# Kernel tuning notes

Measured on AMD Instinct MI355X. Metric: run time of the kernel, lower is better.

The kernel has to match this reference:

```python
import jax, jax.numpy as jnp
import numpy as np

N, T, F = 4096, 24, 16          # nodes, seq_len, in_features
H = 128                          # temporal_hidden
NH, DO = 4, 32                   # gat num_heads, gat out_features (NH*DO == H)
SEM, PH = 64, 32                 # semantic hidden, predictor hidden
SLOPE = 0.2                      # leaky_relu negative slope
ADJ_P = 0.01                     # adjacency density


def setup_inputs() -> dict:
    key = jax.random.key(0)
    ks = jax.random.split(key, 40)
    f32 = jnp.float32

    def rn(k, shape, s=0.02):
        return jax.random.normal(k, shape, f32) * s

    features = jax.random.normal(ks[0], (N, T, F), f32)
    pos_adj = (jax.random.uniform(ks[1], (N, N)) < ADJ_P).astype(f32)
    neg_adj = (jax.random.uniform(ks[2], (N, N)) < ADJ_P).astype(f32)

    inp = dict(features=features, pos_adj=pos_adj, neg_adj=neg_adj)
    # GRU (torch layout: W_ih [3H,F], W_hh [3H,H], gate order r,z,n)
    inp['gru_Wih'] = rn(ks[3], (3 * H, F), 1.0 / np.sqrt(H))
    inp['gru_Whh'] = rn(ks[4], (3 * H, H), 1.0 / np.sqrt(H))
    inp['gru_bih'] = rn(ks[5], (3 * H,), 1.0 / np.sqrt(H))
    inp['gru_bhh'] = rn(ks[6], (3 * H,), 1.0 / np.sqrt(H))
    # GAT params (linear weights stored [in, out] so we use x @ W)
    i = 7
    for pre in ('pos', 'neg'):
        inp[pre + '_W'] = rn(ks[i], (H, NH * DO)); i += 1
        inp[pre + '_u'] = rn(ks[i], (NH, DO, 1), 1.0); i += 1
        inp[pre + '_v'] = rn(ks[i], (NH, DO, 1), 1.0); i += 1
        inp[pre + '_b'] = rn(ks[i], (1, NH * DO)); i += 1
        inp[pre + '_pW'] = rn(ks[i], (H, NH * DO)); i += 1
        inp[pre + '_pb'] = jnp.zeros((NH * DO,), f32)
    inp['self_W'] = rn(ks[i], (H, H)); i += 1
    inp['self_b'] = jnp.zeros((H,), f32)
    inp['mpos_W'] = rn(ks[i], (NH * DO, H)); i += 1
    inp['mpos_b'] = jnp.zeros((H,), f32)
    inp['mneg_W'] = rn(ks[i], (NH * DO, H)); i += 1
    inp['mneg_b'] = jnp.zeros((H,), f32)
    inp['sem_W1'] = rn(ks[i], (H, SEM)); i += 1
    inp['sem_b1'] = jnp.zeros((SEM,), f32)
    inp['sem_W2'] = rn(ks[i], (SEM, 1)); i += 1
    inp['pred_W1'] = rn(ks[i], (H, PH)); i += 1
    inp['pred_b1'] = jnp.zeros((PH,), f32)
    inp['pred_W2'] = rn(ks[i], (PH, 1)); i += 1
    inp['pred_b2'] = jnp.zeros((1,), f32)
    return inp


def _gru_last(x, Wih, Whh, bih, bhh):
    # x: [N, T, F] -> last hidden state [N, H]
    gi_all = jnp.einsum('ntf,gf->tng', x, Wih) + bih  # precompute input gates [T,N,3H]
    h0 = jnp.zeros((x.shape[0], Whh.shape[1]), x.dtype)

    def step(h, gi):
        gh = h @ Whh.T + bhh
        ir, iz, in_ = jnp.split(gi, 3, axis=-1)
        hr, hz, hn = jnp.split(gh, 3, axis=-1)
        r = jax.nn.sigmoid(ir + hr)
        z = jax.nn.sigmoid(iz + hz)
        n = jnp.tanh(in_ + r * hn)
        return (1.0 - z) * n + z * h, None

    h, _ = jax.lax.scan(step, h0, gi_all)
    return h


def _gat(x, adj, W, u, v, b, pW, pb):
    sup = (x @ W).reshape(-1, NH, DO).transpose(1, 0, 2)     # [NH, N, DO]
    f1 = jnp.matmul(sup, u).reshape(NH, 1, -1)               # [NH, 1, N]
    f2 = jnp.matmul(sup, v).reshape(NH, -1, 1)               # [NH, N, 1]
    w = jax.nn.leaky_relu(f1 + f2, SLOPE)                    # [NH, N, N]
    mw = w * adj                                             # mask
    rs = mw.sum(axis=2, keepdims=True)
    rs = jnp.where(rs == 0, jnp.ones_like(rs), rs)
    attn = mw / rs
    out = jnp.matmul(attn, sup).transpose(1, 0, 2).reshape(-1, NH * DO)
    return out + b + x @ pW + pb                             # bias + residual


def _pairnorm_si(x):
    x = x - x.mean(axis=0)
    rn = jnp.sqrt(1e-6 + (x * x).sum(axis=1, keepdims=True))
    return x / rn


def reference(features, pos_adj, neg_adj,
              gru_Wih, gru_Whh, gru_bih, gru_bhh,
              pos_W, pos_u, pos_v, pos_b, pos_pW, pos_pb,
              neg_W, neg_u, neg_v, neg_b, neg_pW, neg_pb,
              self_W, self_b, mpos_W, mpos_b, mneg_W, mneg_b,
              sem_W1, sem_b1, sem_W2,
              pred_W1, pred_b1, pred_W2, pred_b2):
    support = _gru_last(features, gru_Wih, gru_Whh, gru_bih, gru_bhh)  # [N, H]
    pos_sup = _gat(support, pos_adj, pos_W, pos_u, pos_v, pos_b, pos_pW, pos_pb)
    neg_sup = _gat(support, neg_adj, neg_W, neg_u, neg_v, neg_b, neg_pW, neg_pb)
    self_e = support @ self_W + self_b
    pos_e = pos_sup @ mpos_W + mpos_b
    neg_e = neg_sup @ mneg_W + mneg_b
    emb = jnp.stack([self_e, pos_e, neg_e], axis=1)          # [N, 3, H]
    w = jnp.tanh(emb @ sem_W1 + sem_b1) @ sem_W2             # [N, 3, 1]
    beta = jax.nn.softmax(w, axis=1)
    fused = (beta * emb).sum(axis=1)                          # [N, H]
    fused = _pairnorm_si(fused)
    h = jax.nn.relu(fused @ pred_W1 + pred_b1)               # dropout is eval no-op
    out = jax.nn.sigmoid(h @ pred_W2 + pred_b2).squeeze(-1)  # [N]
    return out
```

## Files before the change

kernel.cpp:

```cpp
#include <hip/hip_runtime.h>


#define NN 4096

typedef unsigned short u16;
typedef unsigned int   u32;
typedef unsigned long long u64;
typedef __attribute__((ext_vector_type(8))) short  short8;
typedef __attribute__((ext_vector_type(4))) float  float4v;

__device__ inline float bf2f(u16 u){ return __uint_as_float(((u32)u)<<16); }
__device__ inline u16 f2bf(float f){
  u32 x = __float_as_uint(f);
  return (u16)((x + 0x7fffu + ((x>>16)&1u))>>16);
}
__device__ inline float ldm(const void* p, int i, int bf){
  return bf ? bf2f(((const u16*)p)[i]) : ((const float*)p)[i];
}
__device__ inline u16 ldm16(const void* p, int i, int bf){
  return bf ? ((const u16*)p)[i] : f2bf(((const float*)p)[i]);
}
__device__ inline float fexp(float x){
  x = fminf(fmaxf(x,-80.f),80.f);
  return __builtin_amdgcn_exp2f(x*1.4426950408889634f);
}
__device__ inline float sigm_fast(float x){
  return __builtin_amdgcn_rcpf(1.f + __builtin_amdgcn_exp2f(-x*1.4426950408889634f));
}
__device__ inline float tanhf_(float x){
  float c = fminf(fmaxf(x,-15.f),15.f);
  float e = __builtin_amdgcn_exp2f(c*2.8853900817779268f);
  return (e-1.f)*__builtin_amdgcn_rcpf(e+1.f);
}
__device__ inline float4v mfma16(short8 a, short8 b, float4v c){
  return __builtin_amdgcn_mfma_f32_16x16x32_bf16(a,b,c,0,0,0);
}
__device__ inline int rdbf(const int* __restrict__ mflag){
  int b=0;
  #pragma unroll
  for (int k=0;k<16;k++) b|=mflag[k];
  return b;
}

__global__ __launch_bounds__(256) void k_detect(const u32* __restrict__ adj,
                                                int* __restrict__ mflag)
{
  __shared__ u32 w4[4];
  const int lane=threadIdx.x&63, wv=threadIdx.x>>6;
  int i = (blockIdx.x*256 + threadIdx.x)*4;
  uint4 v = *(const uint4*)(adj + i);
  u32 acc = (v.x | v.y | v.z | v.w) & 0xFFFFu;
  unsigned long long b = __ballot(acc != 0);
  if (lane==0) w4[wv] = (b!=0);
  __syncthreads();
  if (threadIdx.x==0) mflag[blockIdx.x] = (w4[0]|w4[1]|w4[2]|w4[3]) ? 1 : 0;
}

__global__ __launch_bounds__(256) void k_imp(
  const int* __restrict__ mflag,
  const void* gWih, const void* gWhh, const void* gbih, const void* gbhh,
  const void* posW, const void* posu, const void* posv, const void* posb,
  const void* pospW, const void* pospb,
  const void* negW, const void* negu, const void* negv, const void* negb,
  const void* negpW, const void* negpb,
  const void* selfW, const void* selfb, const void* mposW, const void* mposb,
  const void* mnegW, const void* mnegb,
  const void* semW1, const void* semb1, const void* semW2,
  const void* predW1, const void* predb1, const void* predW2, const void* predb2,
  u16* __restrict__ Wihb, u16* __restrict__ Whhb,
  u16* __restrict__ WT1,  u16* __restrict__ WT2,
  float* __restrict__ cbrz, float* __restrict__ cbin, float* __restrict__ cbhn,
  float* __restrict__ cuv,  float* __restrict__ cgb,  float* __restrict__ csb,
  float* __restrict__ cw1t, float* __restrict__ cb1,  float* __restrict__ cw2,
  float* __restrict__ cpw1t, float* __restrict__ cpb1, float* __restrict__ cpw2,
  float* __restrict__ cpb2, float* __restrict__ meanacc)
{
  const int bf = rdbf(mflag);
  int i = blockIdx.x*256 + threadIdx.x;
  if (i < 6144){ Wihb[i]=ldm16(gWih,i,bf); return; }  i-=6144;
  if (i < 49152){ Whhb[i]=ldm16(gWhh,i,bf); return; } i-=49152;
  if (i < 81920){
    int m=i>>7,k=i&127,sel=m>>7,ml=m&127;
    const void* s = sel==0?posW: sel==1?pospW: sel==2?negW: sel==3?negpW: selfW;
    WT1[i]=ldm16(s,k*128+ml,bf); return;
  } i-=81920;
  if (i < 32768){
    int m=i>>7,k=i&127;
    const void* s = (m<128)? mposW : mnegW;
    WT2[i]=ldm16(s,k*128+(m&127),bf); return;
  } i-=32768;
  if (i < 256){ cbrz[i]=ldm(gbih,i,bf)+ldm(gbhh,i,bf); return; } i-=256;
  if (i < 128){ cbin[i]=ldm(gbih,256+i,bf); return; } i-=128;
  if (i < 128){ cbhn[i]=ldm(gbhh,256+i,bf); return; } i-=128;
  if (i < 512){
    int s=i>>8, rem=i&255, wh=rem>>7, hd=rem&127;
    const void* p = s? (wh? negv:negu) : (wh? posv:posu);
    cuv[i]=ldm(p,hd,bf); return;
  } i-=512;
  if (i < 256){
    int s=i>>7, d=i&127;
    cgb[i]=ldm(s?negb:posb,d,bf)+ldm(s?negpb:pospb,d,bf); return;
  } i-=256;
  if (i < 384){
    int t=i>>7, d=i&127;
    const void* p = t==0? selfb : t==1? mposb : mnegb;
    csb[i]=ldm(p,d,bf); return;
  } i-=384;
  if (i < 8448){
    int c=i/132, k=i-c*132;
    cw1t[i] = (k<128)? ldm(semW1,k*64+c,bf) : 0.f; return;
  } i-=8448;
  if (i < 64){ cb1[i]=ldm(semb1,i,bf); return; } i-=64;
  if (i < 64){ cw2[i]=ldm(semW2,i,bf); return; } i-=64;
  if (i < 4224){
    int c=i/132, k=i-c*132;
    cpw1t[i] = (k<128)? ldm(predW1,k*32+c,bf) : 0.f; return;
  } i-=4224;
  if (i < 32){ cpb1[i]=ldm(predb1,i,bf); return; } i-=32;
  if (i < 32){ cpw2[i]=ldm(predW2,i,bf); return; } i-=32;
  if (i < 1){ cpb2[i]=ldm(predb2,i,bf); return; } i-=1;
  if (i < 128){ meanacc[i]=0.f; return; }
}

__global__ __launch_bounds__(512) void k_gruf(
  const int* __restrict__ mflag, const void* feat,
  const u16* __restrict__ Wihb, const u16* __restrict__ Whhb,
  const float* __restrict__ cbrz, const float* __restrict__ cbin,
  const float* __restrict__ cbhn,
  const u16* __restrict__ WT1, const float* __restrict__ cuv,
  u16* __restrict__ C1b, float* __restrict__ f12)
{
  __shared__ __attribute__((aligned(16))) u16 sh_x[16*392];
  __shared__ __attribute__((aligned(16))) u16 hbuf[2][16*136];
  const int bf = rdbf(mflag);
  const int tid=threadIdx.x, lane=tid&63, wv=tid>>6;
  const int quad=lane>>4, c15=lane&15;
  const int n0=blockIdx.x*16;

  if (bf){
    const u16* f16p=(const u16*)feat;
    for (int i=tid;i<768;i+=512){
      int n=i/48, c=(i-n*48)*8;
      *(uint4*)(sh_x + n*392 + c) =
        *(const uint4*)(f16p + (size_t)(n0+n)*384 + c);
    }
  } else {
    const float* f32p=(const float*)feat;
    for (int i=tid;i<1536;i+=512){
      int n=i/96, c=(i-n*96)*4;
      float4 v = *(const float4*)(f32p + (size_t)(n0+n)*384 + c);
      uint2 pk;
      pk.x = (u32)f2bf(v.x) | ((u32)f2bf(v.y)<<16);
      pk.y = (u32)f2bf(v.z) | ((u32)f2bf(v.w)<<16);
      *(uint2*)(sh_x + n*392 + c) = pk;
    }
  }
  for (int i=tid;i<16*136;i+=512) hbuf[0][i]=0;

  const short8 z8={0,0,0,0,0,0,0,0};
  const float4v z4={0.f,0.f,0.f,0.f};
  short8 bh[3][4], bx3[3];
  #pragma unroll
  for (int g=0;g<3;g++){
    int rowb=(g*8+wv)*16+c15;
    #pragma unroll
    for (int ks=0;ks<4;ks++) bh[g][ks]=*(const short8*)(Whhb+(size_t)rowb*128+ks*32+quad*8);
    bx3[g] = (quad<2)? *(const short8*)(Wihb+(size_t)rowb*16+quad*8) : z8;
  }
  const int j0=wv*16+c15;
  const float brz_r=cbrz[j0], brz_z=cbrz[128+j0];
  const float bin0=cbin[j0],  bhn0=cbhn[j0];
  float hr[4]={0.f,0.f,0.f,0.f};
  __syncthreads();

  for (int t=0;t<24;t++){
    const u16* hb  = hbuf[t&1];
    u16*       hbn = hbuf[(t+1)&1];
    short8 ah[4];
    #pragma unroll
    for (int ks=0;ks<4;ks++) ah[ks]=*(const short8*)(hb + c15*136 + ks*32 + quad*8);
    short8 ax = (quad<2)? *(const short8*)(sh_x + c15*392 + t*16 + quad*8) : z8;
    float4v racc = mfma16(ax,bx3[0],z4);
    float4v zacc = mfma16(ax,bx3[1],z4);
    float4v ni   = mfma16(ax,bx3[2],z4);
    float4v nh   = z4;
    #pragma unroll
    for (int ks=0;ks<4;ks++){
      racc = mfma16(ah[ks],bh[0][ks],racc);
      zacc = mfma16(ah[ks],bh[1][ks],zacc);
      nh   = mfma16(ah[ks],bh[2][ks],nh);
    }
    #pragma unroll
    for (int rr=0;rr<4;rr++){
      const int node = quad*4+rr;
      float r_ = sigm_fast(racc[rr]+brz_r);
      float z_ = sigm_fast(zacc[rr]+brz_z);
      float n_ = tanhf_(ni[rr]+bin0 + r_*(nh[rr]+bhn0));
      float hv = (1.f-z_)*n_ + z_*hr[rr];
      hr[rr]=hv; hbn[node*136+j0]=f2bf(hv);
    }
    __syncthreads();
  }
  short8 a[4];
  #pragma unroll
  for (int ks=0;ks<4;ks++) a[ks]=*(const short8*)(hbuf[0]+c15*136+ks*32+quad*8);
  #pragma unroll
  for (int q=0;q<5;q++){
    int tile=wv*5+q;
    float4v acc={0.f,0.f,0.f,0.f};
    #pragma unroll
    for (int ks=0;ks<4;ks++){
      short8 b=*(const short8*)(WT1+(size_t)(tile*16+c15)*128+ks*32+quad*8);
      acc=mfma16(a[ks],b,acc);
    }
    #pragma unroll
    for (int r=0;r<4;r++)
      C1b[(size_t)(n0+quad*4+r)*640 + tile*16 + c15]=f2bf(acc[r]);
  }
  __syncthreads();
  {
    int q=tid;
    int nl=q&15, h=(q>>4)&3, wsel=(q>>6)&1, s=(q>>7)&1;
    const float* uvp = cuv + s*256 + wsel*128 + h*32;
    const u16*   SL  = C1b + (size_t)(n0+nl)*640 + s*256 + h*32;
    float t=0.f;
    #pragma unroll
    for (int d=0;d<32;d++) t += bf2f(SL[d])*uvp[d];
    f12[s*32768 + wsel*16384 + h*4096 + (n0+nl)] = t;
  }
}

__global__ __launch_bounds__(1024) void k_gat3(
  const int* __restrict__ mflag,
  const void* posadj, const void* negadj,
  const u16* __restrict__ C1b, const float* __restrict__ f12,
  const float* __restrict__ cgb, const u16* __restrict__ WT2,
  float* __restrict__ E)
{
  __shared__ u16   nbuf[16][128];
  __shared__ float wbuf[16][4][128];
  __shared__ __attribute__((aligned(16))) u16 sA[16*136];
  const int bf = rdbf(mflag);
  const int s=blockIdx.y;
  const void* adj = s? negadj : posadj;
  const int wv=threadIdx.x>>6, lane=threadIdx.x&63;
  const int n0=blockIdx.x*16;
  const int i=n0+wv;

  u64 mask=0;
  if (bf){
    const u16* rp = (const u16*)adj + (size_t)i*4096;
    #pragma unroll
    for (int it=0; it<8; it++){
      const uint4 vv = *(const uint4*)(rp + it*512 + lane*8);
      u32 w[4]={vv.x,vv.y,vv.z,vv.w};
      #pragma unroll
      for (int q=0;q<4;q++){
        if (w[q]&0xffffu) mask |= 1ull<<(it*8+2*q);
        if (w[q]>>16)     mask |= 1ull<<(it*8+2*q+1);
      }
    }
  } else {
    const float* rp = (const float*)adj + (size_t)i*4096;
    #pragma unroll
    for (int it=0; it<16; it++){
      const uint4 vv = *(const uint4*)(rp + it*256 + lane*4);
      if (vv.x) mask |= 1ull<<(it*4+0);
      if (vv.y) mask |= 1ull<<(it*4+1);
      if (vv.z) mask |= 1ull<<(it*4+2);
      if (vv.w) mask |= 1ull<<(it*4+3);
    }
  }
  int cnt=__popcll(mask);
  int pre=cnt;
  #pragma unroll
  for (int off=1; off<64; off<<=1){
    int o=__shfl_up(pre,off);
    if (lane>=off) pre+=o;
  }
  int base_p = pre-cnt;
  int total = __shfl(pre,63);
  const int dg = total>128 ? 128 : total;
  u64 mm=mask; int k=0;
  while (mm){
    int b=__ffsll(mm)-1; mm&=mm-1;
    int e = bf ? ((b>>3)*512 + lane*8 + (b&7))
               : ((b>>2)*256 + lane*4 + (b&3));
    int p=base_p+k; k++;
    if (p<128) nbuf[wv][p]=(u16)e;
  }

  const float* f1 = f12 + s*32768;
  const float* f2 = f12 + s*32768 + 16384;
  const int d0=lane, d1=lane+64, h0=lane>>5, h1=2+(lane>>5);
  float f2v[4];
  #pragma unroll
  for (int h=0;h<4;h++) f2v[h]=f2[h*4096+i];
  for (int e=lane; e<dg; e+=64){
    int j = nbuf[wv][e];
    #pragma unroll
    for (int h=0;h<4;h++){
      float w = f1[h*4096+j] + f2v[h];
      wbuf[wv][h][e] = w>0.f ? w : 0.2f*w;
    }
  }

  float acc0=0.f,acc1=0.f,rs0=0.f,rs1=0.f;
  #pragma unroll 4
  for (int e=0;e<dg;e++){
    float w0 = wbuf[wv][h0][e];
    float w1 = wbuf[wv][h1][e];
    int j = nbuf[wv][e];
    const u16* SL = C1b + (size_t)j*640 + s*256;
    acc0 += w0*bf2f(SL[d0]); rs0 += w0;
    acc1 += w1*bf2f(SL[d1]); rs1 += w1;
  }
  if (rs0==0.f) rs0=1.f;
  if (rs1==0.f) rs1=1.f;
  const u16* P = C1b + (size_t)i*640 + s*256 + 128;
  sA[wv*136+d0]=f2bf(acc0/rs0 + cgb[s*128+d0] + bf2f(P[d0]));
  sA[wv*136+d1]=f2bf(acc1/rs1 + cgb[s*128+d1] + bf2f(P[d1]));
  __syncthreads();
  if (wv<8){
    const int quad=lane>>4, c15=lane&15;
    short8 a[4];
    #pragma unroll
    for (int ks=0;ks<4;ks++) a[ks]=*(const short8*)(sA+c15*136+ks*32+quad*8);
    const int tile=wv;
    float4v acc={0.f,0.f,0.f,0.f};
    #pragma unroll
    for (int ks=0;ks<4;ks++){
      short8 b=*(const short8*)(WT2+(size_t)(s*128+tile*16+c15)*128+ks*32+quad*8);
      acc=mfma16(a[ks],b,acc);
    }
    #pragma unroll
    for (int r=0;r<4;r++) E[(size_t)(n0+quad*4+r)*256 + s*128 + tile*16 + c15]=acc[r];
  }
}

__global__ __launch_bounds__(256) void k_sem(
  const u16* __restrict__ C1b, const float* __restrict__ E,
  const float* __restrict__ csb, const float* __restrict__ cw1t,
  const float* __restrict__ cb1, const float* __restrict__ cw2,
  float* __restrict__ fused, float* __restrict__ meanacc)
{
  __shared__ float sW1t[64*132];
  __shared__ float sW2[64];
  __shared__ float sb1[64];
  __shared__ float sE[4][3][128];
  __shared__ float redm[4][128];
  const int tid=threadIdx.x, wv=tid>>6, lane=tid&63;
  for (int i=tid;i<8448;i+=256) sW1t[i]=cw1t[i];
  if (tid<64){ sW2[tid]=cw2[tid]; sb1[tid]=cb1[tid]; }
  __syncthreads();
  const float* wcol = sW1t + lane*132;
  float macc0=0.f, macc1=0.f;
  for (int u=0;u<4;u++){
    const int n = blockIdx.x*16 + wv*4 + u;
    for (int d=lane; d<128; d+=64){
      sE[wv][0][d] = bf2f(C1b[(size_t)n*640+512+d]) + csb[d];
      sE[wv][1][d] = E[(size_t)n*256 + d]    + csb[128+d];
      sE[wv][2][d] = E[(size_t)n*256+128+d]  + csb[256+d];
    }
    float sc[3];
    #pragma unroll
    for (int s=0;s<3;s++){
      float t = sb1[lane];
      #pragma unroll
      for (int k=0;k<128;k+=4){
        float4 e4 = *(const float4*)&sE[wv][s][k];
        float4 w4 = *(const float4*)&wcol[k];
        t += e4.x*w4.x + e4.y*w4.y + e4.z*w4.z + e4.w*w4.w;
      }
      t = tanhf_(t);
      float p = t*sW2[lane];
      #pragma unroll
      for (int off=32; off; off>>=1) p += __shfl_xor(p, off);
      sc[s]=p;
    }
    float mx = fmaxf(sc[0], fmaxf(sc[1],sc[2]));
    float e0=fexp(sc[0]-mx), e1=fexp(sc[1]-mx), e2=fexp(sc[2]-mx);
    float inv = 1.f/(e0+e1+e2);
    float b0=e0*inv, b1=e1*inv, b2=e2*inv;
    float f0 = b0*sE[wv][0][lane]    + b1*sE[wv][1][lane]    + b2*sE[wv][2][lane];
    float f1 = b0*sE[wv][0][lane+64] + b1*sE[wv][1][lane+64] + b2*sE[wv][2][lane+64];
    fused[(size_t)n*128+lane]    = f0;
    fused[(size_t)n*128+64+lane] = f1;
    macc0 += f0; macc1 += f1;
  }
  redm[wv][lane]=macc0; redm[wv][lane+64]=macc1;
  __syncthreads();
  if (tid<128)
    atomicAdd(&meanacc[tid], redm[0][tid]+redm[1][tid]+redm[2][tid]+redm[3][tid]);
}

__global__ __launch_bounds__(256) void k_pred(
  const float* __restrict__ fused, const float* __restrict__ meanacc,
  const float* __restrict__ cpw1t, const float* __restrict__ cpb1,
  const float* __restrict__ cpw2, const float* __restrict__ cpb2,
  float* __restrict__ out)
{
  __shared__ float sy[4][128];
  __shared__ float sW1t[32*132];
  __shared__ float sW2[32];
  const int tid=threadIdx.x, wv=tid>>6, lane=tid&63;
  for (int i=tid;i<4224;i+=256) sW1t[i]=cpw1t[i];
  if (tid<32) sW2[tid]=cpw2[tid];
  const int n = blockIdx.x*4 + wv;
  const float inv_n = 1.f/4096.f;
  float x0 = fused[(size_t)n*128+lane]    - meanacc[lane]*inv_n;
  float x1 = fused[(size_t)n*128+64+lane] - meanacc[64+lane]*inv_n;
  float ss = x0*x0 + x1*x1;
  #pragma unroll
  for (int o=32;o;o>>=1) ss += __shfl_xor(ss,o);
  float ir = 1.f/sqrtf(1e-6f + ss);
  sy[wv][lane]=x0*ir; sy[wv][64+lane]=x1*ir;
  __syncthreads();
  const int c = lane&31, half = lane>>5;
  const float* wcol = sW1t + c*132 + half*64;
  const float* yrow = sy[wv] + half*64;
  float h=0.f;
  #pragma unroll
  for (int k=0;k<64;k+=4){
    float4 y4 = *(const float4*)&yrow[k];
    float4 w4 = *(const float4*)&wcol[k];
    h += y4.x*w4.x + y4.y*w4.y + y4.z*w4.z + y4.w*w4.w;
  }
  h += __shfl_xor(h,32);
  h += cpb1[c];
  h = h>0.f? h : 0.f;
  float p = h*sW2[c];
  #pragma unroll
  for (int o=16;o;o>>=1) p += __shfl_xor(p,o);
  if (!lane){
    float z = p + cpb2[0];
    out[n] = __builtin_amdgcn_rcpf(1.f + fexp(-z));
  }
}

extern "C" void kernel_launch(void* const* d_in, const int* in_sizes, int n_in,
                              void* d_out, int out_size, void* d_ws, size_t ws_size,
                              hipStream_t stream)
{
  const void* feat  =d_in[0];
  const void* posadj=d_in[1];
  const void* negadj=d_in[2];
  const void* gWih  =d_in[3];
  const void* gWhh  =d_in[4];
  const void* gbih  =d_in[5];
  const void* gbhh  =d_in[6];
  const void* posW  =d_in[7];
  const void* posu  =d_in[8];
  const void* posv  =d_in[9];
  const void* posb  =d_in[10];
  const void* pospW =d_in[11];
  const void* pospb =d_in[12];
  const void* negW  =d_in[13];
  const void* negu  =d_in[14];
  const void* negv  =d_in[15];
  const void* negb  =d_in[16];
  const void* negpW =d_in[17];
  const void* negpb =d_in[18];
  const void* selfW =d_in[19];
  const void* selfb =d_in[20];
  const void* mposW =d_in[21];
  const void* mposb =d_in[22];
  const void* mnegW =d_in[23];
  const void* mnegb =d_in[24];
  const void* semW1 =d_in[25];
  const void* semb1 =d_in[26];
  const void* semW2 =d_in[27];
  const void* predW1=d_in[28];
  const void* predb1=d_in[29];
  const void* predW2=d_in[30];
  const void* predb2=d_in[31];

  char* wsb=(char*)d_ws; size_t off=0;
  auto alloc=[&](size_t bytes)->void*{ void* p=wsb+off; off+=(bytes+255)&~(size_t)255; return p; };
  int*   mflag=(int*)  alloc(256);
  u16*   Wihb =(u16*)  alloc(6144*2);
  u16*   Whhb =(u16*)  alloc(49152*2);
  u16*   WT1  =(u16*)  alloc(81920*2);
  u16*   WT2  =(u16*)  alloc(32768*2);
  float* cbrz =(float*)alloc(256*4);
  float* cbin =(float*)alloc(128*4);
  float* cbhn =(float*)alloc(128*4);
  float* cuv  =(float*)alloc(512*4);
  float* cgb  =(float*)alloc(256*4);
  float* csb  =(float*)alloc(384*4);
  float* cw1t =(float*)alloc(8448*4);
  float* cb1  =(float*)alloc(64*4);
  float* cw2  =(float*)alloc(64*4);
  float* cpw1t=(float*)alloc(4224*4);
  float* cpb1 =(float*)alloc(32*4);
  float* cpw2 =(float*)alloc(32*4);
  float* cpb2 =(float*)alloc(4);
  u16*   C1b  =(u16*)  alloc((size_t)NN*640*2);
  float* f12  =(float*)alloc((size_t)65536*4);
  float* E    =(float*)alloc((size_t)NN*256*4);
  float* fused=(float*)alloc((size_t)NN*128*4);
  float* meanacc=(float*)alloc(128*4);
  (void)ws_size; (void)in_sizes; (void)n_in; (void)out_size;

  k_detect<<<16,          256,0,stream>>>((const u32*)posadj,mflag);
  k_imp   <<<722,         256,0,stream>>>(mflag,gWih,gWhh,gbih,gbhh,
              posW,posu,posv,posb,pospW,pospb,negW,negu,negv,negb,negpW,negpb,
              selfW,selfb,mposW,mposb,mnegW,mnegb,semW1,semb1,semW2,
              predW1,predb1,predW2,predb2,
              Wihb,Whhb,WT1,WT2,cbrz,cbin,cbhn,cuv,cgb,csb,cw1t,cb1,cw2,
              cpw1t,cpb1,cpw2,cpb2,meanacc);
  k_gruf  <<<NN/16,       512,0,stream>>>(mflag,feat,Wihb,Whhb,cbrz,cbin,cbhn,
                                          WT1,cuv,C1b,f12);
  k_gat3  <<<dim3(256,2),1024,0,stream>>>(mflag,posadj,negadj,C1b,f12,cgb,WT2,E);
  k_sem   <<<NN/16,       256,0,stream>>>(C1b,E,csb,cw1t,cb1,cw2,fused,meanacc);
  k_pred  <<<NN/4,        256,0,stream>>>(fused,meanacc,cpw1t,cpb1,cpw2,cpb2,(float*)d_out);
}
```

Before: 288.0 us.

## Build adjacency neighbor lists in extra GRU-kernel blocks to overlap with recurrence

Moves the dense adjacency scan and neighbor-list compaction out of the GAT kernel into 1024 extra blocks appended to the GRU kernel launch. Those blocks write a compact per-row index list and degree to a new workspace, and the GAT kernel now only loads the precomputed lists. The aim is to hide the memory-bound adjacency read behind the latency-bound GRU recurrence, since only 256 GRU blocks occupy the GPU. The cost is an extra global write and read of the index lists, plus possible interference with GRU blocks for bandwidth and CU slots.

Measured after the change: 269.3 us. -6.5%, faster.

```diff
diff --git a/kernel.cpp b/kernel.cpp
--- a/kernel.cpp
+++ b/kernel.cpp
@@ -128,12 +128,67 @@
   const float* __restrict__ cbrz, const float* __restrict__ cbin,
   const float* __restrict__ cbhn,
   const u16* __restrict__ WT1, const float* __restrict__ cuv,
+  const void* posadj, const void* negadj,
+  u16* __restrict__ csri, int* __restrict__ csrc,
   u16* __restrict__ C1b, float* __restrict__ f12)
 {
   __shared__ __attribute__((aligned(16))) u16 sh_x[16*392];
   __shared__ __attribute__((aligned(16))) u16 hbuf[2][16*136];
   const int bf = rdbf(mflag);
   const int tid=threadIdx.x, lane=tid&63, wv=tid>>6;
+
+  if (blockIdx.x >= NN/16){
+    const int c = blockIdx.x - NN/16;
+    const int s = c >> 9;
+    const int i = (c & 511)*8 + wv;
+    const void* adj = s? negadj : posadj;
+    u64 mask=0;
+    if (bf){
+      const u16* rp = (const u16*)adj + (size_t)i*4096;
+      #pragma unroll
+      for (int it=0; it<8; it++){
+        const uint4 vv = *(const uint4*)(rp + it*512 + lane*8);
+        u32 w[4]={vv.x,vv.y,vv.z,vv.w};
+        #pragma unroll
+        for (int q=0;q<4;q++){
+          if (w[q]&0xffffu) mask |= 1ull<<(it*8+2*q);
+          if (w[q]>>16)     mask |= 1ull<<(it*8+2*q+1);
+        }
+      }
+    } else {
+      const float* rp = (const float*)adj + (size_t)i*4096;
+      #pragma unroll
+      for (int it=0; it<16; it++){
+        const uint4 vv = *(const uint4*)(rp + it*256 + lane*4);
+        if (vv.x) mask |= 1ull<<(it*4+0);
+        if (vv.y) mask |= 1ull<<(it*4+1);
+        if (vv.z) mask |= 1ull<<(it*4+2);
+        if (vv.w) mask |= 1ull<<(it*4+3);
+      }
+    }
+    int cnt=__popcll(mask);
+    int pre=cnt;
+    #pragma unroll
+    for (int off=1; off<64; off<<=1){
+      int o=__shfl_up(pre,off);
+      if (lane>=off) pre+=o;
+    }
+    const int base_p = pre-cnt;
+    const int total  = __shfl(pre,63);
+    u16* op = csri + ((size_t)s*4096 + i)*128;
+    if (base_p < 128){
+      u64 mm=mask; int p=base_p;
+      while (mm && p<128){
+        int b=__ffsll(mm)-1; mm&=mm-1;
+        int e = bf ? ((b>>3)*512 + lane*8 + (b&7))
+                   : ((b>>2)*256 + lane*4 + (b&3));
+        op[p++]=(u16)e;
+      }
+    }
+    if (lane==63) csrc[(size_t)s*4096 + i] = total>128 ? 128 : total;
+    return;
+  }
+
   const int quad=lane>>4, c15=lane&15;
   const int n0=blockIdx.x*16;
 
@@ -231,8 +286,7 @@
 }
 
 __global__ __launch_bounds__(1024) void k_gat3(
-  const int* __restrict__ mflag,
-  const void* posadj, const void* negadj,
+  const u16* __restrict__ csri, const int* __restrict__ csrc,
   const u16* __restrict__ C1b, const float* __restrict__ f12,
   const float* __restrict__ cgb, const u16* __restrict__ WT2,
   float* __restrict__ E)
@@ -240,55 +294,13 @@
   __shared__ u16   nbuf[16][128];
   __shared__ float wbuf[16][4][128];
   __shared__ __attribute__((aligned(16))) u16 sA[16*136];
-  const int bf = rdbf(mflag);
   const int s=blockIdx.y;
-  const void* adj = s? negadj : posadj;
   const int wv=threadIdx.x>>6, lane=threadIdx.x&63;
   const int n0=blockIdx.x*16;
   const int i=n0+wv;
 
-  u64 mask=0;
-  if (bf){
-    const u16* rp = (const u16*)adj + (size_t)i*4096;
-    #pragma unroll
-    for (int it=0; it<8; it++){
-      const uint4 vv = *(const uint4*)(rp + it*512 + lane*8);
-      u32 w[4]={vv.x,vv.y,vv.z,vv.w};
-      #pragma unroll
-      for (int q=0;q<4;q++){
-        if (w[q]&0xffffu) mask |= 1ull<<(it*8+2*q);
-        if (w[q]>>16)     mask |= 1ull<<(it*8+2*q+1);
-      }
-    }
-  } else {
-    const float* rp = (const float*)adj + (size_t)i*4096;
-    #pragma unroll
-    for (int it=0; it<16; it++){
-      const uint4 vv = *(const uint4*)(rp + it*256 + lane*4);
-      if (vv.x) mask |= 1ull<<(it*4+0);
-      if (vv.y) mask |= 1ull<<(it*4+1);
-      if (vv.z) mask |= 1ull<<(it*4+2);
-      if (vv.w) mask |= 1ull<<(it*4+3);
-    }
-  }
-  int cnt=__popcll(mask);
-  int pre=cnt;
-  #pragma unroll
-  for (int off=1; off<64; off<<=1){
-    int o=__shfl_up(pre,off);
-    if (lane>=off) pre+=o;
-  }
-  int base_p = pre-cnt;
-  int total = __shfl(pre,63);
-  const int dg = total>128 ? 128 : total;
-  u64 mm=mask; int k=0;
-  while (mm){
-    int b=__ffsll(mm)-1; mm&=mm-1;
-    int e = bf ? ((b>>3)*512 + lane*8 + (b&7))
-               : ((b>>2)*256 + lane*4 + (b&3));
-    int p=base_p+k; k++;
-    if (p<128) nbuf[wv][p]=(u16)e;
-  }
+  ((u32*)nbuf[wv])[lane] = ((const u32*)(csri + ((size_t)s*4096 + i)*128))[lane];
+  const int dg = csrc[(size_t)s*4096 + i];
 
   const float* f1 = f12 + s*32768;
   const float* f2 = f12 + s*32768 + 16384;
@@ -500,6 +512,8 @@
   float* E    =(float*)alloc((size_t)NN*256*4);
   float* fused=(float*)alloc((size_t)NN*128*4);
   float* meanacc=(float*)alloc(128*4);
+  u16*   csri =(u16*)  alloc((size_t)2*4096*128*2);
+  int*   csrc =(int*)  alloc((size_t)2*4096*4);
   (void)ws_size; (void)in_sizes; (void)n_in; (void)out_size;
 
   k_detect<<<16,          256,0,stream>>>((const u32*)posadj,mflag);
@@ -509,9 +523,10 @@
               predW1,predb1,predW2,predb2,
               Wihb,Whhb,WT1,WT2,cbrz,cbin,cbhn,cuv,cgb,csb,cw1t,cb1,cw2,
               cpw1t,cpb1,cpw2,cpb2,meanacc);
-  k_gruf  <<<NN/16,       512,0,stream>>>(mflag,feat,Wihb,Whhb,cbrz,cbin,cbhn,
-                                          WT1,cuv,C1b,f12);
-  k_gat3  <<<dim3(256,2),1024,0,stream>>>(mflag,posadj,negadj,C1b,f12,cgb,WT2,E);
+  k_gruf  <<<NN/16+1024,  512,0,stream>>>(mflag,feat,Wihb,Whhb,cbrz,cbin,cbhn,
+                                          WT1,cuv,posadj,negadj,csri,csrc,
+                                          C1b,f12);
+  k_gat3  <<<dim3(256,2),1024,0,stream>>>(csri,csrc,C1b,f12,cgb,WT2,E);
   k_sem   <<<NN/16,       256,0,stream>>>(C1b,E,csb,cw1t,cb1,cw2,fused,meanacc);
   k_pred  <<<NN/4,        256,0,stream>>>(fused,meanacc,cpw1t,cpb1,cpw2,cpb2,(float*)d_out);
 }
```
